# Performance work log

Measured on AMD Instinct MI355X. Metric: run time of the kernel, lower is better.

## Reference

```python
import jax, jax.numpy as jnp
import numpy as np

D_MODEL = 512
D_INNER = 1024  # expand * d_model
D_STATE = 128
D_CONV = 4
DT_RANK = 32
DT_MIN, DT_MAX, DT_FLOOR = 0.001, 0.1, 1e-4


def setup_inputs() -> dict:
    key = jax.random.key(0)
    ks = jax.random.split(key, 8)
    B, S = 2, 1024
    return {
        "x": jax.random.normal(ks[0], (B, S, D_MODEL), jnp.float32),
        "W_in": jax.random.normal(ks[1], (D_MODEL, 2 * D_INNER), jnp.float32) * 0.02,
        "conv_w": jax.random.normal(ks[2], (D_INNER, 1, D_CONV), jnp.float32) * 0.1,
        "conv_b": jnp.zeros((D_INNER,), jnp.float32),
        "W_x": jax.random.normal(ks[3], (D_INNER, DT_RANK + 2 * D_STATE), jnp.float32) * 0.02,
        "W_dt": jax.random.normal(ks[4], (DT_RANK, D_INNER), jnp.float32) * 0.02,
        "b_dt": jnp.zeros((D_INNER,), jnp.float32),
        "W_out": jax.random.normal(ks[5], (D_INNER, D_MODEL), jnp.float32) * 0.02,
    }


def _mamba_forward(x, W_in, conv_w, conv_b, W_x, W_dt, b_dt, W_out):
    Bsz, S, _ = x.shape
    xr = x @ W_in                              # [B,S,2*d_inner]
    xs, res = jnp.split(xr, 2, axis=-1)        # each [B,S,d_inner]

    # depthwise causal conv (torch pads both sides by d_conv-1 then truncates
    # to seq_len, which equals a left-pad-only causal conv)
    xc = xs.transpose(0, 2, 1)                 # [B,d_inner,S]
    xc = jax.lax.conv_general_dilated(
        xc, conv_w, window_strides=(1,), padding=[(D_CONV - 1, 0)],
        feature_group_count=D_INNER)
    u = (xc + conv_b[None, :, None]).transpose(0, 2, 1)  # [B,S,d_inner]

    dbl = u @ W_x                              # [B,S,dt_rank+2*d_state]
    dt, Bm, Cm = jnp.split(dbl, [DT_RANK, DT_RANK + D_STATE], axis=-1)
    dt = dt @ W_dt + b_dt                      # [B,S,d_inner]
    dt = jnp.clip(jax.nn.softplus(dt + DT_FLOOR), DT_MIN, DT_MAX)

    # selective scan: h_t = h_{t-1}*(1-dt_t) + x_t (outer) B_t ; y_t = h_t . C_t
    def step(h, inp):
        x_t, dt_t, B_t, C_t = inp              # [B,d_inner],[B,d_inner],[B,N],[B,N]
        h = h * (1.0 - dt_t)[..., None] + x_t[..., None] * B_t[:, None, :]
        y = jnp.einsum('bdn,bn->bd', h, C_t)
        return h, y

    h0 = jnp.zeros((Bsz, D_INNER, D_STATE), u.dtype)
    xs_t = (u.transpose(1, 0, 2), dt.transpose(1, 0, 2),
            Bm.transpose(1, 0, 2), Cm.transpose(1, 0, 2))
    _, ys = jax.lax.scan(step, h0, xs_t)       # ys: [S,B,d_inner]

    y = ys.transpose(1, 0, 2) + res
    return y @ W_out                           # [B,S,d_model]


def reference(x, W_in, conv_w, conv_b, W_x, W_dt, b_dt, W_out):
    return _mamba_forward(x, W_in, conv_w, conv_b, W_x, W_dt, b_dt, W_out)
```

## Files before the change

### kernel.cpp

```cpp
#include <hip/hip_runtime.h>
#include <math.h>

#define S_LEN 1024
#define BATCH 2
#define DM 512
#define DI 1024
#define DS 128
#define DTR 32
#define CL 64
#define NC (S_LEN / CL)

typedef unsigned short ushortT;
typedef __attribute__((ext_vector_type(8))) short short8;
typedef __attribute__((ext_vector_type(4))) float f32x4;

__device__ __forceinline__ ushortT f2b(float f) {
  unsigned u = __builtin_bit_cast(unsigned, f);
  unsigned r = (u + 0x7fff + ((u >> 16) & 1)) >> 16;
  return (ushortT)r;
}
__device__ __forceinline__ float b2f(ushortT h) {
  return __builtin_bit_cast(float, (unsigned)h << 16);
}

#define GLOAD16(g, l)                                                     \
  __builtin_amdgcn_global_load_lds(                                       \
      (const __attribute__((address_space(1))) void*)(g),                 \
      (__attribute__((address_space(3))) void*)(l), 16, 0, 0)

template<int MODE>
__global__ __launch_bounds__(256) void gemm_mfma(
    const ushortT* __restrict__ A, const ushortT* __restrict__ Bt,
    void* __restrict__ Cout, int N, int K, int ldc, int nbx) {
  __shared__ ushortT As[128 * 32];
  __shared__ ushortT Bs[128 * 32];
  const int nwg = gridDim.x;
  const int bid = blockIdx.x;
  const int flat = (bid & 7) * (nwg >> 3) + (bid >> 3);
  const int bxi = flat % nbx, byi = flat / nbx;
  const int bm = byi * 128, bn = bxi * 128;
  const int tid = threadIdx.x;
  const int l = tid & 63, w = tid >> 6;
  const int wr = w >> 1, wc = w & 1;
  const int srow = l >> 2, scol = (l & 3) * 8;
  f32x4 acc[4][4] = {};
  for (int k0 = 0; k0 < K; k0 += 32) {
#pragma unroll
    for (int j = 0; j < 2; ++j) {
      int sub = w * 2 + j;
      const ushortT* gA = A + (size_t)(bm + sub * 16 + srow) * K + k0 + scol;
      GLOAD16(gA, &As[sub * 512]);
      const ushortT* gB = Bt + (size_t)(bn + sub * 16 + srow) * K + k0 + scol;
      GLOAD16(gB, &Bs[sub * 512]);
    }
    __syncthreads();
    short8 a[4], b[4];
#pragma unroll
    for (int m = 0; m < 4; ++m)
      a[m] = *(const short8*)&As[(wr * 64 + m * 16 + (l & 15)) * 32 + (l >> 4) * 8];
#pragma unroll
    for (int n = 0; n < 4; ++n)
      b[n] = *(const short8*)&Bs[(wc * 64 + n * 16 + (l & 15)) * 32 + (l >> 4) * 8];
#pragma unroll
    for (int m = 0; m < 4; ++m)
#pragma unroll
      for (int n = 0; n < 4; ++n)
        acc[m][n] = __builtin_amdgcn_mfma_f32_16x16x32_bf16(a[m], b[n], acc[m][n], 0, 0, 0);
    __syncthreads();
  }
#pragma unroll
  for (int m = 0; m < 4; ++m) {
    int grow = bm + wr * 64 + m * 16 + (l >> 4) * 4;
#pragma unroll
    for (int n = 0; n < 4; ++n) {
      int gcol = bn + wc * 64 + n * 16 + (l & 15);
      if (gcol >= N) continue;
#pragma unroll
      for (int i = 0; i < 4; ++i) {
        float v = acc[m][n][i];
        if (MODE == 1)
          ((ushortT*)Cout)[(size_t)(grow + i) * ldc + gcol] = f2b(v);
        else
          ((float*)Cout)[(size_t)(grow + i) * ldc + gcol] = v;
      }
    }
  }
}

template<int MODE>
__global__ __launch_bounds__(256) void gemm64(
    const ushortT* __restrict__ A, const ushortT* __restrict__ Bt,
    void* __restrict__ Cout, int N, int K, int ldc, int nbx) {
  __shared__ ushortT As[64 * 32];
  __shared__ ushortT Bs[64 * 32];
  const int nwg = gridDim.x;
  const int bid = blockIdx.x;
  const int flat = (bid & 7) * (nwg >> 3) + (bid >> 3);
  const int bxi = flat % nbx, byi = flat / nbx;
  const int bm = byi * 64, bn = bxi * 64;
  const int tid = threadIdx.x;
  const int l = tid & 63, w = tid >> 6;
  const int wr = w >> 1, wc = w & 1;
  const int srow = tid >> 2, scol = (tid & 3) * 8;
  f32x4 acc[2][2] = {};
  for (int k0 = 0; k0 < K; k0 += 32) {
    GLOAD16(A + (size_t)(bm + srow) * K + k0 + scol, &As[(size_t)tid * 8]);
    GLOAD16(Bt + (size_t)(bn + srow) * K + k0 + scol, &Bs[(size_t)tid * 8]);
    __syncthreads();
    short8 a[2], b[2];
#pragma unroll
    for (int m = 0; m < 2; ++m)
      a[m] = *(const short8*)&As[(wr * 32 + m * 16 + (l & 15)) * 32 + (l >> 4) * 8];
#pragma unroll
    for (int n = 0; n < 2; ++n)
      b[n] = *(const short8*)&Bs[(wc * 32 + n * 16 + (l & 15)) * 32 + (l >> 4) * 8];
#pragma unroll
    for (int m = 0; m < 2; ++m)
#pragma unroll
      for (int n = 0; n < 2; ++n)
        acc[m][n] = __builtin_amdgcn_mfma_f32_16x16x32_bf16(a[m], b[n], acc[m][n], 0, 0, 0);
    __syncthreads();
  }
#pragma unroll
  for (int m = 0; m < 2; ++m) {
    int grow = bm + wr * 32 + m * 16 + (l >> 4) * 4;
#pragma unroll
    for (int n = 0; n < 2; ++n) {
      int gcol = bn + wc * 32 + n * 16 + (l & 15);
      if (gcol >= N) continue;
#pragma unroll
      for (int i = 0; i < 4; ++i) {
        float v = acc[m][n][i];
        if (MODE == 1)
          ((ushortT*)Cout)[(size_t)(grow + i) * ldc + gcol] = f2b(v);
        else
          ((float*)Cout)[(size_t)(grow + i) * ldc + gcol] = v;
      }
    }
  }
}

__global__ __launch_bounds__(256) void prep_all(
    const float* __restrict__ W_in, const float* __restrict__ W_x,
    const float* __restrict__ W_out, const float* __restrict__ x,
    ushortT* __restrict__ Wt_in, ushortT* __restrict__ Wt_x,
    ushortT* __restrict__ Wt_out, ushortT* __restrict__ x_bf) {
  __shared__ float tb[32][33];
  int bid = blockIdx.x;
  int tx = threadIdx.x, ty = threadIdx.y;
  const float* in; ushortT* out; int K, N, bx, by;
  if (bid < 1024)      { in = W_in;  out = Wt_in;  K = 512;  N = 2048; bx = bid & 63; by = bid >> 6; }
  else if (bid < 1408) { int t2 = bid - 1024; in = W_x;   out = Wt_x;   K = 1024; N = 288;  bx = t2 % 12; by = t2 / 12; }
  else if (bid < 1920) { int t2 = bid - 1408; in = W_out; out = Wt_out; K = 1024; N = 512;  bx = t2 % 16; by = t2 / 16; }
  else {
    int i = (bid - 1920) * 256 + ty * 32 + tx;
    float4 v = ((const float4*)x)[i];
    ushort4 o; o.x = f2b(v.x); o.y = f2b(v.y); o.z = f2b(v.z); o.w = f2b(v.w);
    ((ushort4*)x_bf)[i] = o;
    return;
  }
  int n0 = bx * 32, k0 = by * 32;
  if (n0 < N) {
#pragma unroll
    for (int i = 0; i < 4; ++i)
      tb[ty + 8 * i][tx] = in[(size_t)(k0 + ty + 8 * i) * N + n0 + tx];
    __syncthreads();
#pragma unroll
    for (int i = 0; i < 4; ++i)
      out[(size_t)(n0 + ty + 8 * i) * K + k0 + tx] = f2b(tb[tx][ty + 8 * i]);
  } else {
#pragma unroll
    for (int i = 0; i < 4; ++i)
      out[(size_t)(n0 + ty + 8 * i) * K + k0 + tx] = 0;
  }
}

__global__ __launch_bounds__(256) void conv_kernel(
    const ushortT* __restrict__ xr, const float* __restrict__ w,
    const float* __restrict__ b, ushortT* __restrict__ u) {
  int idx = blockIdx.x * blockDim.x + threadIdx.x;
  int g = idx & 255;
  int s = (idx >> 8) & (S_LEN - 1);
  int bb = idx >> 18;
  int d = g * 4;
  float4 bias = *(const float4*)&b[d];
  float4 w0 = *(const float4*)&w[(d + 0) * 4];
  float4 w1 = *(const float4*)&w[(d + 1) * 4];
  float4 w2 = *(const float4*)&w[(d + 2) * 4];
  float4 w3 = *(const float4*)&w[(d + 3) * 4];
  float a0 = bias.x, a1 = bias.y, a2 = bias.z, a3 = bias.w;
  const ushortT* xs = xr + (size_t)(bb * S_LEN) * (2 * DI) + d;
#pragma unroll
  for (int k = 0; k < 4; ++k) {
    int si = s - 3 + k;
    if (si >= 0) {
      ushort4 v = *(const ushort4*)&xs[(size_t)si * (2 * DI)];
      float wk0 = ((const float*)&w0)[k], wk1 = ((const float*)&w1)[k];
      float wk2 = ((const float*)&w2)[k], wk3 = ((const float*)&w3)[k];
      a0 = fmaf(b2f(v.x), wk0, a0);
      a1 = fmaf(b2f(v.y), wk1, a1);
      a2 = fmaf(b2f(v.z), wk2, a2);
      a3 = fmaf(b2f(v.w), wk3, a3);
    }
  }
  ushort4 o; o.x = f2b(a0); o.y = f2b(a1); o.z = f2b(a2); o.w = f2b(a3);
  *(ushort4*)&u[(size_t)idx * 4] = o;
}

__global__ __launch_bounds__(256) void megachunk(
    const float* __restrict__ dbl, const float* __restrict__ W_dt,
    const float* __restrict__ b_dt, const ushortT* __restrict__ u_bf,
    float* __restrict__ D, ushortT* __restrict__ ut,
    ushortT* __restrict__ zb) {
  __shared__ ushortT Btl[128][72];
  __shared__ float   Dl[64][66];
  __shared__ ushortT utl[64][72];
  __shared__ float   dtl[64][36];
  __shared__ ushortT Wl[32][68];
  const int t = threadIdx.x;
  const int dg = blockIdx.x, bc = blockIdx.y;
  const int b = bc >> 4, c = bc & 15;
  const size_t rowbase = (size_t)(b * S_LEN + c * CL) * DI + dg * 64;

#pragma unroll
  for (int j = 0; j < 8; ++j) {
    int idx4 = j * 256 + t;
    int s = idx4 >> 5, n4 = (idx4 & 31) * 4;
    float4 v = *(const float4*)&dbl[(size_t)(bc * 64 + s) * 288 + 32 + n4];
    Btl[n4][s] = f2b(v.x); Btl[n4 + 1][s] = f2b(v.y);
    Btl[n4 + 2][s] = f2b(v.z); Btl[n4 + 3][s] = f2b(v.w);
  }
#pragma unroll
  for (int j = 0; j < 2; ++j) {
    int idx4 = j * 256 + t;
    int s = idx4 >> 3, k4 = (idx4 & 7) * 4;
    *(float4*)&dtl[s][k4] = *(const float4*)&dbl[(size_t)(bc * 64 + s) * 288 + k4];
  }
#pragma unroll
  for (int j = 0; j < 4; ++j) {
    int idx2 = j * 256 + t;
    int k = idx2 >> 5, d2 = (idx2 & 31) * 2;
    float2 v = *(const float2*)&W_dt[(size_t)k * DI + dg * 64 + d2];
    Wl[k][d2] = f2b(v.x); Wl[k][d2 + 1] = f2b(v.y);
  }
  __syncthreads();

  {
    int d = t & 63, sq = t >> 6;
    float wreg[32];
#pragma unroll
    for (int k = 0; k < 32; ++k) wreg[k] = b2f(Wl[k][d]);
    float bias = b_dt[dg * 64 + d] + 1e-4f;
#pragma unroll 4
    for (int j = 0; j < 16; ++j) {
      int s = sq * 16 + j;
      float acc = bias;
#pragma unroll
      for (int k = 0; k < 32; ++k) acc = fmaf(dtl[s][k], wreg[k], acc);
      acc = (acc > 20.f) ? acc : log1pf(expf(acc));
      acc = fminf(fmaxf(acc, 0.001f), 0.1f);
      Dl[d][s] = 1.f - acc;
    }
  }
  __syncthreads();

  if (t < 64) {
    float cum = 1.f;
#pragma unroll 16
    for (int s = 0; s < CL; ++s) { cum *= Dl[t][s]; Dl[t][s] = cum; }
  }
  __syncthreads();

#pragma unroll
  for (int j = 0; j < 4; ++j) {
    int idx4 = j * 256 + t;
    int s = idx4 >> 4, d4 = (idx4 & 15) * 4;
    float4 v;
    v.x = Dl[d4][s]; v.y = Dl[d4 + 1][s]; v.z = Dl[d4 + 2][s]; v.w = Dl[d4 + 3][s];
    *(float4*)&D[rowbase + (size_t)s * DI + d4] = v;
  }
#pragma unroll
  for (int j = 0; j < 2; ++j) {
    int idx8 = j * 256 + t;
    int s = idx8 >> 3, d8 = (idx8 & 7) * 8;
    float4 raw = *(const float4*)&u_bf[rowbase + (size_t)s * DI + d8];
    const ushortT* up = (const ushortT*)&raw;
#pragma unroll
    for (int k = 0; k < 8; ++k)
      utl[d8 + k][s] = f2b(b2f(up[k]) / Dl[d8 + k][s]);
  }
  __syncthreads();

#pragma unroll
  for (int j = 0; j < 2; ++j) {
    int idx8 = j * 256 + t;
    int d = idx8 >> 3, s8 = (idx8 & 7) * 8;
    float4 v; ushortT* vp = (ushortT*)&v;
#pragma unroll
    for (int k = 0; k < 8; ++k) vp[k] = utl[d][s8 + k];
    *(float4*)&ut[((size_t)bc * DI + dg * 64 + d) * CL + s8] = v;
  }

  {
    const int l = t & 63, w = t >> 6;
    f32x4 acc[8] = {};
#pragma unroll
    for (int kk = 0; kk < 2; ++kk) {
      short8 a = *(const short8*)&utl[w * 16 + (l & 15)][kk * 32 + (l >> 4) * 8];
#pragma unroll
      for (int n = 0; n < 8; ++n) {
        short8 bb = *(const short8*)&Btl[n * 16 + (l & 15)][kk * 32 + (l >> 4) * 8];
        acc[n] = __builtin_amdgcn_mfma_f32_16x16x32_bf16(a, bb, acc[n], 0, 0, 0);
      }
    }
#pragma unroll
    for (int n = 0; n < 8; ++n) {
      int gn = n * 16 + (l & 15);
#pragma unroll
      for (int i = 0; i < 4; ++i) {
        int d = dg * 64 + w * 16 + (l >> 4) * 4 + i;
        zb[(((size_t)(b * DI + d)) * NC + c) * 128 + gn] = f2b(acc[n][i]);
      }
    }
  }
}

__global__ __launch_bounds__(256) void scan_pass2(
    const ushortT* __restrict__ zb, const float* __restrict__ D,
    ushortT* __restrict__ hstb) {
  int wid = (blockIdx.x * blockDim.x + threadIdx.x) >> 6;
  int lane = threadIdx.x & 63;
  int b = wid >> 10, d = wid & (DI - 1);
  size_t base = (size_t)wid * NC * 128;
  float h0 = 0.f, h1 = 0.f;
#pragma unroll
  for (int c = 0; c < NC; ++c) {
    float dend = D[((size_t)(b * S_LEN + c * CL + CL - 1)) * DI + d];
    ushort2 z2 = *(const ushort2*)&zb[base + c * 128 + 2 * lane];
    ushort2 he;
    he.x = f2b(h0); he.y = f2b(h1);
    *(ushort2*)&hstb[base + c * 128 + 2 * lane] = he;
    h0 = dend * (h0 + b2f(z2.x));
    h1 = dend * (h1 + b2f(z2.y));
  }
}

__global__ __launch_bounds__(256) void gemm_y(
    const float* __restrict__ dbl, const ushortT* __restrict__ ut,
    const ushortT* __restrict__ hstb, const float* __restrict__ D,
    const ushortT* __restrict__ xr_bf, ushortT* __restrict__ yr) {
  __shared__ ushortT Bl[64][136];
  __shared__ ushortT Cl[64][136];
  __shared__ ushortT Gl[64][72];
  const int tid = threadIdx.x;
  const int l = tid & 63, w = tid >> 6;
  const int bc = blockIdx.y, d0 = blockIdx.x * 64;
  const int b = bc >> 4, c = bc & 15;
  const int brow = b * S_LEN + c * CL;
#pragma unroll
  for (int j = 0; j < 16; ++j) {
    int idx4 = j * 256 + tid;
    int row = idx4 >> 6, c4 = (idx4 & 63) * 4;
    float4 v = *(const float4*)&dbl[(size_t)(bc * 64 + row) * 288 + 32 + c4];
    ushortT o0 = f2b(v.x), o1 = f2b(v.y), o2 = f2b(v.z), o3 = f2b(v.w);
    if (c4 < 128) { Bl[row][c4] = o0; Bl[row][c4+1] = o1; Bl[row][c4+2] = o2; Bl[row][c4+3] = o3; }
    else { int cc = c4 - 128; Cl[row][cc] = o0; Cl[row][cc+1] = o1; Cl[row][cc+2] = o2; Cl[row][cc+3] = o3; }
  }
  __syncthreads();
  {
    f32x4 gacc[4] = {};
#pragma unroll
    for (int kk = 0; kk < 4; ++kk) {
      short8 a = *(const short8*)&Cl[w * 16 + (l & 15)][kk * 32 + (l >> 4) * 8];
#pragma unroll
      for (int nf = 0; nf < 4; ++nf) {
        short8 bb = *(const short8*)&Bl[nf * 16 + (l & 15)][kk * 32 + (l >> 4) * 8];
        gacc[nf] = __builtin_amdgcn_mfma_f32_16x16x32_bf16(a, bb, gacc[nf], 0, 0, 0);
      }
    }
#pragma unroll
    for (int nf = 0; nf < 4; ++nf) {
      int s = nf * 16 + (l & 15);
#pragma unroll
      for (int i = 0; i < 4; ++i) {
        int tr = w * 16 + (l >> 4) * 4 + i;
        Gl[tr][s] = f2b((s <= tr) ? gacc[nf][i] : 0.f);
      }
    }
  }
  __syncthreads();
  f32x4 acc[4] = {};
#pragma unroll
  for (int kk = 0; kk < 2; ++kk) {
    short8 a = *(const short8*)&Gl[w * 16 + (l & 15)][kk * 32 + (l >> 4) * 8];
#pragma unroll
    for (int n = 0; n < 4; ++n) {
      int d = d0 + n * 16 + (l & 15);
      short8 bb = *(const short8*)&ut[((size_t)bc * DI + d) * CL + kk * 32 + (l >> 4) * 8];
      acc[n] = __builtin_amdgcn_mfma_f32_16x16x32_bf16(a, bb, acc[n], 0, 0, 0);
    }
  }
#pragma unroll
  for (int kk = 0; kk < 4; ++kk) {
    short8 a = *(const short8*)&Cl[w * 16 + (l & 15)][kk * 32 + (l >> 4) * 8];
#pragma unroll
    for (int n = 0; n < 4; ++n) {
      int d = d0 + n * 16 + (l & 15);
      short8 bb = *(const short8*)&hstb[((size_t)(b * DI + d)) * (NC * 128) + c * 128 + kk * 32 + (l >> 4) * 8];
      acc[n] = __builtin_amdgcn_mfma_f32_16x16x32_bf16(a, bb, acc[n], 0, 0, 0);
    }
  }
#pragma unroll
  for (int n = 0; n < 4; ++n) {
    int d = d0 + n * 16 + (l & 15);
#pragma unroll
    for (int i = 0; i < 4; ++i) {
      int gr = brow + w * 16 + (l >> 4) * 4 + i;
      float Dv = D[(size_t)gr * DI + d];
      float res = b2f(xr_bf[(size_t)gr * 2048 + 1024 + d]);
      yr[(size_t)gr * DI + d] = f2b(acc[n][i] * Dv + res);
    }
  }
}

extern "C" void kernel_launch(void* const* d_in, const int* in_sizes, int n_in,
                              void* d_out, int out_size, void* d_ws, size_t ws_size,
                              hipStream_t stream) {
  const float* x      = (const float*)d_in[0];
  const float* W_in   = (const float*)d_in[1];
  const float* conv_w = (const float*)d_in[2];
  const float* conv_b = (const float*)d_in[3];
  const float* W_x    = (const float*)d_in[4];
  const float* W_dt   = (const float*)d_in[5];
  const float* b_dt   = (const float*)d_in[6];
  const float* W_out  = (const float*)d_in[7];
  float* out = (float*)d_out;
  float* ws = (float*)d_ws;

  ushortT* xr_bf = (ushortT*)ws;
  ushortT* u_bf  = (ushortT*)(ws + 2097152);
  float*   dbl   = ws + 3145728;
  float*   Dc    = ws + 3735552;
  ushortT* ut    = (ushortT*)(ws + 5832704);
  ushortT* zb    = (ushortT*)(ws + 6881280);
  ushortT* hstb  = (ushortT*)(ws + 8978432);
  ushortT* x_bf  = (ushortT*)(ws + 11075584);
  ushortT* Wt_in = (ushortT*)(ws + 11599872);
  ushortT* Wt_x  = (ushortT*)(ws + 12124160);
  ushortT* Wt_out= (ushortT*)(ws + 12320768);
  ushortT* yr_bf = (ushortT*)(ws + 12582912);

  dim3 blk(256);
  prep_all<<<2944, dim3(32, 8), 0, stream>>>(W_in, W_x, W_out, x,
                                             Wt_in, Wt_x, Wt_out, x_bf);
  gemm_mfma<1><<<256, blk, 0, stream>>>(x_bf, Wt_in, xr_bf, 2 * DI, DM, 2 * DI, 16);
  conv_kernel<<<2048, blk, 0, stream>>>(xr_bf, conv_w, conv_b, u_bf);
  gemm64<0><<<160, blk, 0, stream>>>(u_bf, Wt_x, dbl, DTR + 2 * DS, DI, DTR + 2 * DS, 5);
  megachunk<<<dim3(16, 32), blk, 0, stream>>>(dbl, W_dt, b_dt, u_bf, Dc, ut, zb);
  scan_pass2<<<512, blk, 0, stream>>>(zb, Dc, hstb);
  gemm_y<<<dim3(16, 32), blk, 0, stream>>>(dbl, ut, hstb, Dc, xr_bf, yr_bf);
  gemm64<0><<<256, blk, 0, stream>>>(yr_bf, Wt_out, out, DM, DI, DM, 8);
}
```

Measured before the change: 101.7 us.

## Use 64x64 GEMM for input projection, vectorize transpose stores, reorder megachunk

The input projection GEMM switches from a 128x128-tile kernel with 256 blocks to the 64x64-tile gemm64 with 1024 blocks, giving more workgroups across the CUs at the cost of less data reuse per tile. The weight-transpose prep kernel now writes ushort2 pairs instead of scalar bf16 stores to widen global writes. In megachunk, the u/D division and the MFMA chunk-state computation are moved ahead of the D and ut global stores, so compute can overlap with the outstanding writes.

```diff
diff --git a/kernel.cpp b/kernel.cpp
--- a/kernel.cpp
+++ b/kernel.cpp
@@ -27,65 +27,6 @@
   __builtin_amdgcn_global_load_lds(                                       \
       (const __attribute__((address_space(1))) void*)(g),                 \
       (__attribute__((address_space(3))) void*)(l), 16, 0, 0)
-
-template<int MODE>
-__global__ __launch_bounds__(256) void gemm_mfma(
-    const ushortT* __restrict__ A, const ushortT* __restrict__ Bt,
-    void* __restrict__ Cout, int N, int K, int ldc, int nbx) {
-  __shared__ ushortT As[128 * 32];
-  __shared__ ushortT Bs[128 * 32];
-  const int nwg = gridDim.x;
-  const int bid = blockIdx.x;
-  const int flat = (bid & 7) * (nwg >> 3) + (bid >> 3);
-  const int bxi = flat % nbx, byi = flat / nbx;
-  const int bm = byi * 128, bn = bxi * 128;
-  const int tid = threadIdx.x;
-  const int l = tid & 63, w = tid >> 6;
-  const int wr = w >> 1, wc = w & 1;
-  const int srow = l >> 2, scol = (l & 3) * 8;
-  f32x4 acc[4][4] = {};
-  for (int k0 = 0; k0 < K; k0 += 32) {
-#pragma unroll
-    for (int j = 0; j < 2; ++j) {
-      int sub = w * 2 + j;
-      const ushortT* gA = A + (size_t)(bm + sub * 16 + srow) * K + k0 + scol;
-      GLOAD16(gA, &As[sub * 512]);
-      const ushortT* gB = Bt + (size_t)(bn + sub * 16 + srow) * K + k0 + scol;
-      GLOAD16(gB, &Bs[sub * 512]);
-    }
-    __syncthreads();
-    short8 a[4], b[4];
-#pragma unroll
-    for (int m = 0; m < 4; ++m)
-      a[m] = *(const short8*)&As[(wr * 64 + m * 16 + (l & 15)) * 32 + (l >> 4) * 8];
-#pragma unroll
-    for (int n = 0; n < 4; ++n)
-      b[n] = *(const short8*)&Bs[(wc * 64 + n * 16 + (l & 15)) * 32 + (l >> 4) * 8];
-#pragma unroll
-    for (int m = 0; m < 4; ++m)
-#pragma unroll
-      for (int n = 0; n < 4; ++n)
-        acc[m][n] = __builtin_amdgcn_mfma_f32_16x16x32_bf16(a[m], b[n], acc[m][n], 0, 0, 0);
-    __syncthreads();
-  }
-#pragma unroll
-  for (int m = 0; m < 4; ++m) {
-    int grow = bm + wr * 64 + m * 16 + (l >> 4) * 4;
-#pragma unroll
-    for (int n = 0; n < 4; ++n) {
-      int gcol = bn + wc * 64 + n * 16 + (l & 15);
-      if (gcol >= N) continue;
-#pragma unroll
-      for (int i = 0; i < 4; ++i) {
-        float v = acc[m][n][i];
-        if (MODE == 1)
-          ((ushortT*)Cout)[(size_t)(grow + i) * ldc + gcol] = f2b(v);
-        else
-          ((float*)Cout)[(size_t)(grow + i) * ldc + gcol] = v;
-      }
-    }
-  }
-}
 
 template<int MODE>
 __global__ __launch_bounds__(256) void gemm64(
@@ -160,18 +101,29 @@
     return;
   }
   int n0 = bx * 32, k0 = by * 32;
+  int flat = ty * 32 + tx;
   if (n0 < N) {
 #pragma unroll
     for (int i = 0; i < 4; ++i)
       tb[ty + 8 * i][tx] = in[(size_t)(k0 + ty + 8 * i) * N + n0 + tx];
     __syncthreads();
 #pragma unroll
-    for (int i = 0; i < 4; ++i)
-      out[(size_t)(n0 + ty + 8 * i) * K + k0 + tx] = f2b(tb[tx][ty + 8 * i]);
+    for (int j = 0; j < 2; ++j) {
+      int idx = j * 256 + flat;
+      int r = idx >> 4, c2 = idx & 15;
+      ushort2 o;
+      o.x = f2b(tb[2 * c2][r]);
+      o.y = f2b(tb[2 * c2 + 1][r]);
+      *(ushort2*)&out[(size_t)(n0 + r) * K + k0 + 2 * c2] = o;
+    }
   } else {
-#pragma unroll
-    for (int i = 0; i < 4; ++i)
-      out[(size_t)(n0 + ty + 8 * i) * K + k0 + tx] = 0;
+    ushort2 z; z.x = 0; z.y = 0;
+#pragma unroll
+    for (int j = 0; j < 2; ++j) {
+      int idx = j * 256 + flat;
+      int r = idx >> 4, c2 = idx & 15;
+      *(ushort2*)&out[(size_t)(n0 + r) * K + k0 + 2 * c2] = z;
+    }
   }
 }
 
@@ -272,6 +224,41 @@
   __syncthreads();
 
 #pragma unroll
+  for (int j = 0; j < 2; ++j) {
+    int idx8 = j * 256 + t;
+    int s = idx8 >> 3, d8 = (idx8 & 7) * 8;
+    float4 raw = *(const float4*)&u_bf[rowbase + (size_t)s * DI + d8];
+    const ushortT* up = (const ushortT*)&raw;
+#pragma unroll
+    for (int k = 0; k < 8; ++k)
+      utl[d8 + k][s] = f2b(b2f(up[k]) / Dl[d8 + k][s]);
+  }
+  __syncthreads();
+
+  {
+    const int l = t & 63, w = t >> 6;
+    f32x4 acc[8] = {};
+#pragma unroll
+    for (int kk = 0; kk < 2; ++kk) {
+      short8 a = *(const short8*)&utl[w * 16 + (l & 15)][kk * 32 + (l >> 4) * 8];
+#pragma unroll
+      for (int n = 0; n < 8; ++n) {
+        short8 bb = *(const short8*)&Btl[n * 16 + (l & 15)][kk * 32 + (l >> 4) * 8];
+        acc[n] = __builtin_amdgcn_mfma_f32_16x16x32_bf16(a, bb, acc[n], 0, 0, 0);
+      }
+    }
+#pragma unroll
+    for (int n = 0; n < 8; ++n) {
+      int gn = n * 16 + (l & 15);
+#pragma unroll
+      for (int i = 0; i < 4; ++i) {
+        int d = dg * 64 + w * 16 + (l >> 4) * 4 + i;
+        zb[(((size_t)(b * DI + d)) * NC + c) * 128 + gn] = f2b(acc[n][i]);
+      }
+    }
+  }
+
+#pragma unroll
   for (int j = 0; j < 4; ++j) {
     int idx4 = j * 256 + t;
     int s = idx4 >> 4, d4 = (idx4 & 15) * 4;
@@ -282,46 +269,11 @@
 #pragma unroll
   for (int j = 0; j < 2; ++j) {
     int idx8 = j * 256 + t;
-    int s = idx8 >> 3, d8 = (idx8 & 7) * 8;
-    float4 raw = *(const float4*)&u_bf[rowbase + (size_t)s * DI + d8];
-    const ushortT* up = (const ushortT*)&raw;
-#pragma unroll
-    for (int k = 0; k < 8; ++k)
-      utl[d8 + k][s] = f2b(b2f(up[k]) / Dl[d8 + k][s]);
-  }
-  __syncthreads();
-
-#pragma unroll
-  for (int j = 0; j < 2; ++j) {
-    int idx8 = j * 256 + t;
     int d = idx8 >> 3, s8 = (idx8 & 7) * 8;
     float4 v; ushortT* vp = (ushortT*)&v;
 #pragma unroll
     for (int k = 0; k < 8; ++k) vp[k] = utl[d][s8 + k];
     *(float4*)&ut[((size_t)bc * DI + dg * 64 + d) * CL + s8] = v;
-  }
-
-  {
-    const int l = t & 63, w = t >> 6;
-    f32x4 acc[8] = {};
-#pragma unroll
-    for (int kk = 0; kk < 2; ++kk) {
-      short8 a = *(const short8*)&utl[w * 16 + (l & 15)][kk * 32 + (l >> 4) * 8];
-#pragma unroll
-      for (int n = 0; n < 8; ++n) {
-        short8 bb = *(const short8*)&Btl[n * 16 + (l & 15)][kk * 32 + (l >> 4) * 8];
-        acc[n] = __builtin_amdgcn_mfma_f32_16x16x32_bf16(a, bb, acc[n], 0, 0, 0);
-      }
-    }
-#pragma unroll
-    for (int n = 0; n < 8; ++n) {
-      int gn = n * 16 + (l & 15);
-#pragma unroll
-      for (int i = 0; i < 4; ++i) {
-        int d = dg * 64 + w * 16 + (l >> 4) * 4 + i;
-        zb[(((size_t)(b * DI + d)) * NC + c) * 128 + gn] = f2b(acc[n][i]);
-      }
-    }
   }
 }
 
@@ -453,7 +405,7 @@
   dim3 blk(256);
   prep_all<<<2944, dim3(32, 8), 0, stream>>>(W_in, W_x, W_out, x,
                                              Wt_in, Wt_x, Wt_out, x_bf);
-  gemm_mfma<1><<<256, blk, 0, stream>>>(x_bf, Wt_in, xr_bf, 2 * DI, DM, 2 * DI, 16);
+  gemm64<1><<<1024, blk, 0, stream>>>(x_bf, Wt_in, xr_bf, 2 * DI, DM, 2 * DI, 32);
   conv_kernel<<<2048, blk, 0, stream>>>(xr_bf, conv_w, conv_b, u_bf);
   gemm64<0><<<160, blk, 0, stream>>>(u_bf, Wt_x, dbl, DTR + 2 * DS, DI, DTR + 2 * DS, 5);
   megachunk<<<dim3(16, 32), blk, 0, stream>>>(dbl, W_dt, b_dt, u_bf, Dc, ut, zb);
```

Result: faster. 98.17 us (-3.5%).
